# Kernel tuning notes

Hardware: AMD Instinct MI355X
Metric: run time of the kernel (lower is better)

The kernel has to match this reference:

```python
import jax, jax.numpy as jnp
import numpy as np

N = 50000
E = 800000
F_IN = 256
HID = 64
HEADS = 4
CLASSES = 32
NEG_SLOPE = 0.2


def setup_inputs() -> dict:
    key = jax.random.key(0)
    ks = jax.random.split(key, 10)
    x = jax.random.normal(ks[0], (N, F_IN), dtype=jnp.float32)
    edge_index = jax.random.randint(ks[1], (2, E), 0, N, dtype=jnp.int64)
    s1 = 1.0 / np.sqrt(F_IN)
    s2 = 1.0 / np.sqrt(HID * HEADS)
    W1 = jax.random.normal(ks[2], (F_IN, HEADS * HID), dtype=jnp.float32) * s1
    a_src1 = jax.random.normal(ks[3], (HEADS, HID), dtype=jnp.float32) * s1
    a_dst1 = jax.random.normal(ks[4], (HEADS, HID), dtype=jnp.float32) * s1
    b1 = jnp.zeros((HEADS * HID,), dtype=jnp.float32)
    W2 = jax.random.normal(ks[5], (HEADS * HID, CLASSES), dtype=jnp.float32) * s2
    a_src2 = jax.random.normal(ks[6], (1, CLASSES), dtype=jnp.float32) * s2
    a_dst2 = jax.random.normal(ks[7], (1, CLASSES), dtype=jnp.float32) * s2
    b2 = jnp.zeros((CLASSES,), dtype=jnp.float32)
    return {"x": x, "edge_index": edge_index, "W1": W1, "a_src1": a_src1,
            "a_dst1": a_dst1, "b1": b1, "W2": W2, "a_src2": a_src2,
            "a_dst2": a_dst2, "b2": b2}


def gat_conv(x, src, dst, W, a_src, a_dst, bias, num_nodes):
    # PyG GATConv: h = x W, per-head attention logits, segment softmax over dst,
    # scatter-weighted aggregation. src/dst already include self-loops.
    H, C = a_src.shape
    h = (x @ W).reshape(num_nodes, H, C)               # [N, H, C]
    al_s = jnp.sum(h * a_src[None], axis=-1)            # [N, H]
    al_d = jnp.sum(h * a_dst[None], axis=-1)            # [N, H]
    e = jax.nn.leaky_relu(al_s[src] + al_d[dst], NEG_SLOPE)  # [Et, H]
    m = jax.ops.segment_max(e, dst, num_segments=num_nodes)  # [N, H]
    ex = jnp.exp(e - m[dst])
    denom = jax.ops.segment_sum(ex, dst, num_segments=num_nodes)
    alpha = ex / denom[dst]                              # [Et, H]
    out = jax.ops.segment_sum(alpha[:, :, None] * h[src], dst,
                              num_segments=num_nodes)    # [N, H, C]
    return out.reshape(num_nodes, H * C) + bias


def reference(x, edge_index, W1, a_src1, a_dst1, b1, W2, a_src2, a_dst2, b2):
    num_nodes = x.shape[0]
    loop = jnp.arange(num_nodes, dtype=edge_index.dtype)
    src = jnp.concatenate([edge_index[0], loop])  # add_self_loops=True (PyG default)
    dst = jnp.concatenate([edge_index[1], loop])
    # dropout is identity in eval mode
    h = jax.nn.elu(gat_conv(x, src, dst, W1, a_src1, a_dst1, b1, num_nodes))
    out = gat_conv(h, src, dst, W2, a_src2, a_dst2, b2, num_nodes)
    return jax.nn.log_softmax(out, axis=1)
```

## Files before the change

kernel.cpp:

```cpp
#include <hip/hip_runtime.h>
#include <math.h>

#define N_NODES 50000
#define N_EDGES 800000
#define NEG_SLOPE 0.2f
#define PADU N_NODES
#define LOG2E 1.44269504088896f

#define BSHIFT 8
#define NBUK ((N_NODES + 255) >> BSHIFT)
#define BCAP 4608
#define ACHUNK 4096
#define PADBUK 5632
#define ET_PAD_ALLOC (NBUK * PADBUK)

typedef __attribute__((ext_vector_type(8))) short s16x8;
typedef __attribute__((ext_vector_type(4))) float f32x4;
typedef __attribute__((ext_vector_type(2))) float f32x2;

__device__ __forceinline__ unsigned short f2bf(float f) {
    union { float f; unsigned u; } v; v.f = f;
    unsigned r = v.u + 0x7FFF + ((v.u >> 16) & 1);
    return (unsigned short)(r >> 16);
}
__device__ __forceinline__ float asf(unsigned u) {
    union { unsigned u; float f; } v; v.u = u;
    return v.f;
}
__device__ __forceinline__ uint4 pack_bf16_trunc(float4 f0, float4 f1) {
    const unsigned* a = (const unsigned*)&f0;
    const unsigned* b = (const unsigned*)&f1;
    uint4 r;
    r.x = (a[0] >> 16) | (a[1] & 0xffff0000u);
    r.y = (a[2] >> 16) | (a[3] & 0xffff0000u);
    r.z = (b[0] >> 16) | (b[1] & 0xffff0000u);
    r.w = (b[2] >> 16) | (b[3] & 0xffff0000u);
    return r;
}
__device__ __forceinline__ unsigned char f2fp8(float f) {
    return (unsigned char)(__builtin_amdgcn_cvt_pk_fp8_f32(f, f, 0, false) & 0xff);
}


__global__ __launch_bounds__(256) void k_cvtw(const float* __restrict__ W1, const float* __restrict__ W2,
                                              unsigned short* __restrict__ WT, unsigned short* __restrict__ W2T,
                                              int* __restrict__ bcur, float* __restrict__ als1,
                                              unsigned char* __restrict__ H8) {
    int b = blockIdx.x, k = threadIdx.x;
    if (b < 256) {
        WT[b * 256 + k] = f2bf(W1[k * 256 + b]);
    } else if (b < 288) {
        int c = b - 256;
        W2T[c * 256 + k] = f2bf(W2[k * 32 + c]);
    } else {
        if (k < NBUK) bcur[k] = 0;
        if (k >= 196 && k < 200) als1[N_NODES * 4 + (k - 196)] = -1e30f;
        if (k >= 200 && k < 264) ((unsigned*)H8)[(size_t)N_NODES * 64 + (k - 200)] = 0;
    }
}


__global__ __launch_bounds__(256) void k_bin(const int* __restrict__ ei, int* __restrict__ bcur,
                                             unsigned* __restrict__ stage) {
    __shared__ unsigned sdata[ACHUNK];
    __shared__ unsigned short sv[ACHUNK];
    __shared__ int scnt[NBUK];
    __shared__ int soff[NBUK + 1];
    __shared__ int sgbase[NBUK];
    __shared__ int wssc[4];
    int tid = threadIdx.x;
    int e0 = blockIdx.x * ACHUNK;
    int nE = N_EDGES - e0;
    if (nE > ACHUNK) nE = ACHUNK;
    for (int i = tid; i < NBUK; i += 256) scnt[i] = 0;
    __syncthreads();
    for (int i = tid; i < nE; i += 256) {
        int v = ei[N_EDGES + e0 + i];
        sv[i] = (unsigned short)v;
        atomicAdd(&scnt[v >> BSHIFT], 1);
    }
    __syncthreads();
    {
        int lane = tid & 63, w = tid >> 6;
        int val = (tid < NBUK) ? scnt[tid] : 0;
        int incl = val;
        for (int o = 1; o < 64; o <<= 1) {
            int t = __shfl_up(incl, o);
            if (lane >= o) incl += t;
        }
        if (lane == 63) wssc[w] = incl;
        __syncthreads();
        int wb = 0;
        for (int i = 0; i < w; ++i) wb += wssc[i];
        if (tid < NBUK) soff[tid] = wb + incl - val;
        if (tid == 255) soff[NBUK] = wb + incl;
    }
    __syncthreads();
    if (tid < NBUK) {
        int c = scnt[tid];
        sgbase[tid] = c ? atomicAdd(&bcur[tid], c) : 0;
        scnt[tid] = soff[tid];
    }
    __syncthreads();
    for (int i = tid; i < nE; i += 256) {
        int u = ei[e0 + i];
        unsigned v = sv[i];
        int b = (int)(v >> BSHIFT);
        int pos = atomicAdd(&scnt[b], 1);
        sdata[pos] = (unsigned)u | ((v & 255u) << 16) | ((unsigned)b << 24);
    }
    __syncthreads();
    for (int i = tid; i < nE; i += 256) {
        unsigned pk = sdata[i];
        int buk = (int)(pk >> 24);
        int rel = sgbase[buk] + (i - soff[buk]);
        if (rel < BCAP) stage[(size_t)buk * BCAP + rel] = pk;
    }
}


__global__ __launch_bounds__(256) void k_build(const unsigned* __restrict__ stage,
                                               const int* __restrict__ bcur,
                                               int* __restrict__ offp, int* __restrict__ ecnt,
                                               unsigned short* __restrict__ esrc) {
    __shared__ int hist[256];
    __shared__ int lexcl[257];
    __shared__ int ws[4];
    __shared__ int outbuf[PADBUK];
    int b = blockIdx.x, tid = threadIdx.x;
    int n = bcur[b];
    if (n > BCAP) n = BCAP;
    int base = b << BSHIFT;
    int nv = N_NODES - base;
    if (nv > 256) nv = 256;
    hist[tid] = 0;
    __syncthreads();
    const unsigned* sg = stage + (size_t)b * BCAP;
    for (int i = tid; i < n; i += 256) atomicAdd(&hist[(sg[i] >> 16) & 0xFF], 1);
    __syncthreads();
    int lane = tid & 63, w = tid >> 6;
    int c = (tid < nv) ? hist[tid] + 1 : 0;
    int r = (tid < nv) ? ((c + 3) & ~3) : 0;
    int incl = r;
    for (int o = 1; o < 64; o <<= 1) {
        int t = __shfl_up(incl, o);
        if (lane >= o) incl += t;
    }
    if (lane == 63) ws[w] = incl;
    __syncthreads();
    int wb = 0;
    for (int i = 0; i < w; ++i) wb += ws[i];
    int excl = wb + incl - r;
    lexcl[tid] = excl;
    if (tid == 255) lexcl[256] = excl + r;
    int gb = b * PADBUK;
    if (tid < nv) {
        offp[base + tid] = gb + excl;
        ecnt[base + tid] = c;
    }
    __syncthreads();
    int total = lexcl[256];
    if (tid < nv) {
        outbuf[excl] = base + tid;
        for (int j = excl + c; j < excl + r; ++j) outbuf[j] = PADU;
        hist[tid] = 1;
    }
    __syncthreads();
    for (int i = tid; i < n; i += 256) {
        unsigned pk = sg[i];
        int vloc = (int)((pk >> 16) & 0xFF);
        int pos = lexcl[vloc] + atomicAdd(&hist[vloc], 1);
        outbuf[pos] = (int)(pk & 0xffffu);
    }
    __syncthreads();
    for (int i = tid; i < total; i += 256) esrc[gb + i] = (unsigned short)outbuf[i];
}


__global__ __launch_bounds__(256) void k_gemm1m(const float* __restrict__ X, const unsigned short* __restrict__ WT,
                                                const float* __restrict__ a_src, const float* __restrict__ a_dst,
                                                unsigned char* __restrict__ H8,
                                                float* __restrict__ als, float* __restrict__ ald) {
    __shared__ unsigned short As[64][40];
    __shared__ unsigned short Bs[256][40];
    int tid = threadIdx.x;
    int row0 = blockIdx.x * 64;
    int wv = tid >> 6, lane = tid & 63;
    int wm = wv & 1, wn = wv >> 1;
    int lr = lane & 15, quad = lane >> 4;
    f32x4 acc[2][8];
#pragma unroll
    for (int mt = 0; mt < 2; ++mt)
#pragma unroll
        for (int nt = 0; nt < 8; ++nt) acc[mt][nt] = (f32x4){0.f, 0.f, 0.f, 0.f};

    int ar = tid >> 2, aseg = tid & 3;
    for (int k0 = 0; k0 < 256; k0 += 32) {
        {
            int grow = row0 + ar;
            float4 f0 = make_float4(0.f, 0.f, 0.f, 0.f), f1 = f0;
            if (grow < N_NODES) {
                const float* src = X + (size_t)grow * 256 + k0 + aseg * 8;
                f0 = *(const float4*)src;
                f1 = *(const float4*)(src + 4);
            }
            *(uint4*)&As[ar][aseg * 8] = pack_bf16_trunc(f0, f1);
        }
#pragma unroll
        for (int pass = 0; pass < 4; ++pass) {
            int q = tid + pass * 256;
            int n = q >> 2, seg = q & 3;
            uint4 v = *(const uint4*)(WT + (n << 8) + k0 + seg * 8);
            *(uint4*)&Bs[n][seg * 8] = v;
        }
        __syncthreads();
        s16x8 a[2], b[8];
#pragma unroll
        for (int mt = 0; mt < 2; ++mt) a[mt] = *(const s16x8*)&As[wm * 32 + mt * 16 + lr][quad * 8];
#pragma unroll
        for (int nt = 0; nt < 8; ++nt) b[nt] = *(const s16x8*)&Bs[wn * 128 + nt * 16 + lr][quad * 8];
#pragma unroll
        for (int mt = 0; mt < 2; ++mt)
#pragma unroll
            for (int nt = 0; nt < 8; ++nt)
                acc[mt][nt] = __builtin_amdgcn_mfma_f32_16x16x32_bf16(a[mt], b[nt], acc[mt][nt], 0, 0, 0);
        __syncthreads();
    }
#pragma unroll
    for (int mt = 0; mt < 2; ++mt) {
#pragma unroll
        for (int r = 0; r < 4; ++r) {
            int row = row0 + wm * 32 + mt * 16 + quad * 4 + r;
            if (row < N_NODES) {
#pragma unroll
                for (int nt = 0; nt < 8; ++nt) {
                    int col = wn * 128 + nt * 16 + lr;
                    H8[(size_t)row * 256 + col] = f2fp8(acc[mt][nt][r]);
                }
            }
        }
    }
    float av[8], dv[8];
#pragma unroll
    for (int nt = 0; nt < 8; ++nt) {
        int col = wn * 128 + nt * 16 + lr;
        av[nt] = a_src[col] * LOG2E;
        dv[nt] = a_dst[col] * LOG2E;
    }
    float ps[2][8], pd[2][8];
#pragma unroll
    for (int hl = 0; hl < 2; ++hl)
#pragma unroll
        for (int i = 0; i < 8; ++i) { ps[hl][i] = 0.f; pd[hl][i] = 0.f; }
#pragma unroll
    for (int mt = 0; mt < 2; ++mt)
#pragma unroll
        for (int nt = 0; nt < 8; ++nt) {
            int hl = nt >> 2;
#pragma unroll
            for (int r = 0; r < 4; ++r) {
                float v = acc[mt][nt][r];
                ps[hl][mt * 4 + r] = fmaf(v, av[nt], ps[hl][mt * 4 + r]);
                pd[hl][mt * 4 + r] = fmaf(v, dv[nt], pd[hl][mt * 4 + r]);
            }
        }
#pragma unroll
    for (int hl = 0; hl < 2; ++hl)
#pragma unroll
        for (int i = 0; i < 8; ++i) {
            float s = ps[hl][i], d = pd[hl][i];
#pragma unroll
            for (int m = 8; m >= 1; m >>= 1) { s += __shfl_xor(s, m); d += __shfl_xor(d, m); }
            if (lr == 0) {
                int row = row0 + wm * 32 + (i >> 2) * 16 + quad * 4 + (i & 3);
                if (row < N_NODES) {
                    als[row * 4 + wn * 2 + hl] = s;
                    ald[row * 4 + wn * 2 + hl] = d;
                }
            }
        }
}


__global__ __launch_bounds__(256) void k_agg1(const uint2* __restrict__ H8u2,
                                              const float* __restrict__ als, const float* __restrict__ ald_,
                                              const int* __restrict__ offp, const int* __restrict__ ecnt,
                                              const unsigned short* __restrict__ esrc,
                                              const float* __restrict__ b1, uint2* __restrict__ H2p2) {
    int tid = threadIdx.x;
    int wid = (blockIdx.x * 256 + tid) >> 6;
    int half = (tid >> 5) & 1;
    int node = wid * 2 + half;
    int lane = tid & 31;
    int head = lane >> 3;
    float ald = ald_[node * 4 + head];
    int pstart = offp[node];
    int rend = pstart + ((ecnt[node] + 3) & ~3);
    float l = 0.f;
    f32x2 acc0 = (f32x2){0.f, 0.f}, acc1 = (f32x2){0.f, 0.f};
    f32x2 acc2 = (f32x2){0.f, 0.f}, acc3 = (f32x2){0.f, 0.f};

    auto quad = [&](unsigned ua, unsigned ub) {
        int u0 = (int)(ua & 0xffffu), u1 = (int)(ua >> 16);
        int u2 = (int)(ub & 0xffffu), u3 = (int)(ub >> 16);
        uint2 v0 = H8u2[(unsigned)u0 * 32 + lane];
        uint2 v1 = H8u2[(unsigned)u1 * 32 + lane];
        uint2 v2 = H8u2[(unsigned)u2 * 32 + lane];
        uint2 v3 = H8u2[(unsigned)u3 * 32 + lane];
        f32x2 e01 = (f32x2){als[u0 * 4 + head], als[u1 * 4 + head]} + (f32x2){ald, ald};
        f32x2 e23 = (f32x2){als[u2 * 4 + head], als[u3 * 4 + head]} + (f32x2){ald, ald};
        f32x2 t01 = e01 * NEG_SLOPE, t23 = e23 * NEG_SLOPE;
        float e0 = fmaxf(e01.x, t01.x), e1 = fmaxf(e01.y, t01.y);
        float e2 = fmaxf(e23.x, t23.x), e3 = fmaxf(e23.y, t23.y);
        float pw0 = __builtin_amdgcn_exp2f(e0);
        float pw1 = __builtin_amdgcn_exp2f(e1);
        float pw2 = __builtin_amdgcn_exp2f(e2);
        float pw3 = __builtin_amdgcn_exp2f(e3);
        l += (pw0 + pw1) + (pw2 + pw3);
        f32x2 w0 = (f32x2){pw0, pw0}, w1 = (f32x2){pw1, pw1};
        f32x2 w2 = (f32x2){pw2, pw2}, w3 = (f32x2){pw3, pw3};
        acc0 += w0 * __builtin_amdgcn_cvt_pk_f32_fp8(v0.x, false);
        acc1 += w0 * __builtin_amdgcn_cvt_pk_f32_fp8(v0.x, true);
        acc2 += w0 * __builtin_amdgcn_cvt_pk_f32_fp8(v0.y, false);
        acc3 += w0 * __builtin_amdgcn_cvt_pk_f32_fp8(v0.y, true);
        acc0 += w1 * __builtin_amdgcn_cvt_pk_f32_fp8(v1.x, false);
        acc1 += w1 * __builtin_amdgcn_cvt_pk_f32_fp8(v1.x, true);
        acc2 += w1 * __builtin_amdgcn_cvt_pk_f32_fp8(v1.y, false);
        acc3 += w1 * __builtin_amdgcn_cvt_pk_f32_fp8(v1.y, true);
        acc0 += w2 * __builtin_amdgcn_cvt_pk_f32_fp8(v2.x, false);
        acc1 += w2 * __builtin_amdgcn_cvt_pk_f32_fp8(v2.x, true);
        acc2 += w2 * __builtin_amdgcn_cvt_pk_f32_fp8(v2.y, false);
        acc3 += w2 * __builtin_amdgcn_cvt_pk_f32_fp8(v2.y, true);
        acc0 += w3 * __builtin_amdgcn_cvt_pk_f32_fp8(v3.x, false);
        acc1 += w3 * __builtin_amdgcn_cvt_pk_f32_fp8(v3.x, true);
        acc2 += w3 * __builtin_amdgcn_cvt_pk_f32_fp8(v3.y, false);
        acc3 += w3 * __builtin_amdgcn_cvt_pk_f32_fp8(v3.y, true);
    };

    int p = pstart;
    for (; p + 7 < rend; p += 8) {
        uint2 ua = *(const uint2*)(esrc + p);
        uint2 ub = *(const uint2*)(esrc + p + 4);
        quad(ua.x, ua.y);
        quad(ub.x, ub.y);
    }
    if (p < rend) {
        uint2 ua = *(const uint2*)(esrc + p);
        quad(ua.x, ua.y);
    }

    float inv = 1.f / l;
    int c = lane * 8;
    float4 bb0 = *(const float4*)(b1 + c);
    float4 bb1 = *(const float4*)(b1 + c + 4);
    float o0 = acc0.x * inv + bb0.x, o1 = acc0.y * inv + bb0.y;
    float o2 = acc1.x * inv + bb0.z, o3 = acc1.y * inv + bb0.w;
    float o4 = acc2.x * inv + bb1.x, o5 = acc2.y * inv + bb1.y;
    float o6 = acc3.x * inv + bb1.z, o7 = acc3.y * inv + bb1.w;
    o0 = o0 > 0.f ? o0 : expm1f(o0);
    o1 = o1 > 0.f ? o1 : expm1f(o1);
    o2 = o2 > 0.f ? o2 : expm1f(o2);
    o3 = o3 > 0.f ? o3 : expm1f(o3);
    o4 = o4 > 0.f ? o4 : expm1f(o4);
    o5 = o5 > 0.f ? o5 : expm1f(o5);
    o6 = o6 > 0.f ? o6 : expm1f(o6);
    o7 = o7 > 0.f ? o7 : expm1f(o7);
    unsigned pkx = __builtin_amdgcn_cvt_pk_fp8_f32(o0, o1, 0, false);
    pkx = __builtin_amdgcn_cvt_pk_fp8_f32(o2, o3, pkx, true);
    unsigned pky = __builtin_amdgcn_cvt_pk_fp8_f32(o4, o5, 0, false);
    pky = __builtin_amdgcn_cvt_pk_fp8_f32(o6, o7, pky, true);
    H2p2[(unsigned)node * 32 + lane] = make_uint2(pkx, pky);
}


__global__ __launch_bounds__(256) void k_gemm2m(const unsigned* __restrict__ H2p,
                                                const unsigned short* __restrict__ W2T,
                                                const float* __restrict__ as2, const float* __restrict__ ad2,
                                                unsigned short* __restrict__ Gb, float* __restrict__ als2,
                                                float* __restrict__ ald2) {
    int tid = threadIdx.x;
    int wv = tid >> 6, lane = tid & 63, lr = lane & 15, quad = lane >> 4;
    int row0 = blockIdx.x * 64 + wv * 16;
    int rowA = row0 + lr;
    unsigned rA = (rowA < N_NODES) ? (unsigned)rowA : (unsigned)(N_NODES - 1);
    f32x4 acc[2];
    acc[0] = (f32x4){0.f, 0.f, 0.f, 0.f};
    acc[1] = (f32x4){0.f, 0.f, 0.f, 0.f};
#pragma unroll
    for (int k0 = 0; k0 < 256; k0 += 32) {
        uint2 d = *(const uint2*)(H2p + rA * 64 + (k0 >> 2) + quad * 2);
        f32x2 f0 = __builtin_amdgcn_cvt_pk_f32_fp8(d.x, false);
        f32x2 f1 = __builtin_amdgcn_cvt_pk_f32_fp8(d.x, true);
        f32x2 f2 = __builtin_amdgcn_cvt_pk_f32_fp8(d.y, false);
        f32x2 f3 = __builtin_amdgcn_cvt_pk_f32_fp8(d.y, true);
        union { uint4 u; s16x8 s; } cv;
        cv.u = pack_bf16_trunc(make_float4(f0.x, f0.y, f1.x, f1.y), make_float4(f2.x, f2.y, f3.x, f3.y));
        s16x8 afrag = cv.s;
        s16x8 b0 = *(const s16x8*)(W2T + lr * 256 + k0 + quad * 8);
        s16x8 b1f = *(const s16x8*)(W2T + (16 + lr) * 256 + k0 + quad * 8);
        acc[0] = __builtin_amdgcn_mfma_f32_16x16x32_bf16(afrag, b0, acc[0], 0, 0, 0);
        acc[1] = __builtin_amdgcn_mfma_f32_16x16x32_bf16(afrag, b1f, acc[1], 0, 0, 0);
    }
    float a2s = as2[lr] * LOG2E, a2s2 = as2[16 + lr] * LOG2E;
    float a2d = ad2[lr] * LOG2E, a2d2 = ad2[16 + lr] * LOG2E;
#pragma unroll
    for (int r = 0; r < 4; ++r) {
        int row = row0 + quad * 4 + r;
        float g0 = acc[0][r], g1 = acc[1][r];
        float s = g0 * a2s + g1 * a2s2;
        float dd = g0 * a2d + g1 * a2d2;
#pragma unroll
        for (int m = 8; m >= 1; m >>= 1) { s += __shfl_xor(s, m); dd += __shfl_xor(dd, m); }
        if (row < N_NODES) {
            Gb[(size_t)row * 32 + lr] = f2bf(g0);
            Gb[(size_t)row * 32 + 16 + lr] = f2bf(g1);
            if (lr == 0) { als2[row] = s; ald2[row] = dd; }
        }
    }
}


__global__ __launch_bounds__(256) void k_agg2(const unsigned short* __restrict__ Gb,
                                              const float* __restrict__ als2,
                                              const float* __restrict__ ald2_, const int* __restrict__ offp,
                                              const int* __restrict__ ecnt,
                                              const unsigned short* __restrict__ esrc, const float* __restrict__ b2,
                                              float* __restrict__ out) {
    int gid = blockIdx.x * 256 + threadIdx.x;
    int node = gid >> 4;
    int colp = gid & 15;
    if (node >= N_NODES) return;
    float ald = ald2_[node];
    int pstart = offp[node];
    int pend = pstart + ecnt[node];
    float l = 0.f;
    f32x2 accv = (f32x2){0.f, 0.f};

    auto edge1 = [&](int u0) {
        unsigned gpk = *(const unsigned*)(Gb + (size_t)(unsigned)u0 * 32 + 2 * colp);
        f32x2 g01 = (f32x2){asf(gpk << 16), asf(gpk & 0xffff0000u)};
        float e0 = als2[u0] + ald;
        e0 = fmaxf(e0, NEG_SLOPE * e0);
        float pw0 = __builtin_amdgcn_exp2f(e0);
        l += pw0;
        accv += (f32x2){pw0, pw0} * g01;
    };
    auto quad = [&](unsigned ua, unsigned ub) {
        int u0 = (int)(ua & 0xffffu), u1 = (int)(ua >> 16);
        int u2 = (int)(ub & 0xffffu), u3 = (int)(ub >> 16);
        unsigned g0p = *(const unsigned*)(Gb + (size_t)(unsigned)u0 * 32 + 2 * colp);
        unsigned g1p = *(const unsigned*)(Gb + (size_t)(unsigned)u1 * 32 + 2 * colp);
        unsigned g2p = *(const unsigned*)(Gb + (size_t)(unsigned)u2 * 32 + 2 * colp);
        unsigned g3p = *(const unsigned*)(Gb + (size_t)(unsigned)u3 * 32 + 2 * colp);
        f32x2 e01 = (f32x2){als2[u0], als2[u1]} + (f32x2){ald, ald};
        f32x2 e23 = (f32x2){als2[u2], als2[u3]} + (f32x2){ald, ald};
        f32x2 t01 = e01 * NEG_SLOPE, t23 = e23 * NEG_SLOPE;
        float e0 = fmaxf(e01.x, t01.x), e1 = fmaxf(e01.y, t01.y);
        float e2 = fmaxf(e23.x, t23.x), e3 = fmaxf(e23.y, t23.y);
        float pw0 = __builtin_amdgcn_exp2f(e0), pw1 = __builtin_amdgcn_exp2f(e1);
        float pw2 = __builtin_amdgcn_exp2f(e2), pw3 = __builtin_amdgcn_exp2f(e3);
        l += (pw0 + pw1) + (pw2 + pw3);
        f32x2 g0 = (f32x2){asf(g0p << 16), asf(g0p & 0xffff0000u)};
        f32x2 g1 = (f32x2){asf(g1p << 16), asf(g1p & 0xffff0000u)};
        f32x2 g2 = (f32x2){asf(g2p << 16), asf(g2p & 0xffff0000u)};
        f32x2 g3 = (f32x2){asf(g3p << 16), asf(g3p & 0xffff0000u)};
        accv += (f32x2){pw0, pw0} * g0;
        accv += (f32x2){pw1, pw1} * g1;
        accv += (f32x2){pw2, pw2} * g2;
        accv += (f32x2){pw3, pw3} * g3;
    };

    int p = pstart;
    for (; p + 7 < pend; p += 8) {
        uint2 ua = *(const uint2*)(esrc + p);
        uint2 ub = *(const uint2*)(esrc + p + 4);
        quad(ua.x, ua.y);
        quad(ub.x, ub.y);
    }
    for (; p + 3 < pend; p += 4) {
        uint2 ua = *(const uint2*)(esrc + p);
        quad(ua.x, ua.y);
    }
    for (; p < pend; ++p) edge1(esrc[p]);

    float inv = 1.f / l;
    float2 bb = *(const float2*)(b2 + 2 * colp);
    float o0 = accv.x * inv + bb.x;
    float o1 = accv.y * inv + bb.y;
    float mm = fmaxf(o0, o1);
#pragma unroll
    for (int msk = 8; msk >= 1; msk >>= 1) mm = fmaxf(mm, __shfl_xor(mm, msk));
    float s = __expf(o0 - mm) + __expf(o1 - mm);
#pragma unroll
    for (int msk = 8; msk >= 1; msk >>= 1) s += __shfl_xor(s, msk);
    float ls = logf(s);
    float2 res = make_float2(o0 - mm - ls, o1 - mm - ls);
    *(float2*)(out + (size_t)node * 32 + 2 * colp) = res;
}


extern "C" void kernel_launch(void* const* d_in, const int* in_sizes, int n_in,
                              void* d_out, int out_size, void* d_ws, size_t ws_size,
                              hipStream_t stream) {
    const float* x   = (const float*)d_in[0];
    const int*   ei  = (const int*)d_in[1];
    const float* W1  = (const float*)d_in[2];
    const float* as1 = (const float*)d_in[3];
    const float* ad1 = (const float*)d_in[4];
    const float* b1  = (const float*)d_in[5];
    const float* W2  = (const float*)d_in[6];
    const float* as2 = (const float*)d_in[7];
    const float* ad2 = (const float*)d_in[8];
    const float* b2  = (const float*)d_in[9];
    float* out = (float*)d_out;

    char* p = (char*)d_ws;
    auto alloc = [&](size_t bytes) {
        char* r = p;
        p += (bytes + 255) & ~(size_t)255;
        return r;
    };
    unsigned char*  h8  = (unsigned char*)alloc((size_t)(N_NODES + 1) * 256);
    unsigned char*  h2pr= (unsigned char*)alloc((size_t)N_NODES * 64 * 4);
    unsigned short* wt  = (unsigned short*)alloc((size_t)256 * 256 * 2);
    unsigned short* w2t = (unsigned short*)alloc((size_t)32 * 256 * 2);
    float* als1 = (float*)alloc(((size_t)N_NODES * 4 + 4) * 4);
    float* ald1 = (float*)alloc((size_t)N_NODES * 4 * 4);
    float* als2 = (float*)alloc((size_t)N_NODES * 4);
    float* ald2 = (float*)alloc((size_t)N_NODES * 4);
    int* bcur    = (int*)alloc(256 * 4);
    int* offp = (int*)alloc((size_t)N_NODES * 4);
    int* ecnt = (int*)alloc((size_t)N_NODES * 4);
    unsigned short* esrc = (unsigned short*)alloc((size_t)ET_PAD_ALLOC * 2);

    unsigned* stage = (unsigned*)h2pr;
    unsigned* h2p = (unsigned*)h2pr;
    unsigned short* g = (unsigned short*)h8;

    k_cvtw<<<289, 256, 0, stream>>>(W1, W2, wt, w2t, bcur, als1, h8);
    k_bin<<<(N_EDGES + ACHUNK - 1) / ACHUNK, 256, 0, stream>>>(ei, bcur, stage);
    k_build<<<NBUK, 256, 0, stream>>>(stage, bcur, offp, ecnt, esrc);

    k_gemm1m<<<(N_NODES + 63) / 64, 256, 0, stream>>>(x, wt, as1, ad1, h8, als1, ald1);
    k_agg1<<<(N_NODES / 2 + 3) / 4, 256, 0, stream>>>((const uint2*)h8, als1, ald1, offp, ecnt, esrc, b1,
                                                      (uint2*)h2p);
    k_gemm2m<<<(N_NODES + 63) / 64, 256, 0, stream>>>(h2p, w2t, as2, ad2, g, als2, ald2);
    k_agg2<<<(N_NODES * 16 + 255) / 256, 256, 0, stream>>>(g, als2, ald2, offp, ecnt, esrc, b2, out);
}
```

Measured before the change: 216.3 us.

## Merge independent preprocessing kernels into two launches via block-range dispatch

Folds weight conversion into the edge-binning kernel, and the layer-1 GEMM together with the CSR build into a second kernel, so each block picks its role from its block index. Zeroing the bucket counters moves to a hipMemsetAsync. This cuts the launch count from four to two plus a memset, and lets independent work overlap inside a single grid. The cost is a larger shared-memory union for the combined kernel, which may lower occupancy for the GEMM blocks. The GEMM reads the converted weights, but those are written by the previous kernel, so stream ordering still holds.

```diff
diff --git a/kernel.cpp b/kernel.cpp
--- a/kernel.cpp
+++ b/kernel.cpp
@@ -11,8 +11,10 @@
 #define NBUK ((N_NODES + 255) >> BSHIFT)
 #define BCAP 4608
 #define ACHUNK 4096
+#define BINB ((N_EDGES + ACHUNK - 1) / ACHUNK)
 #define PADBUK 5632
 #define ET_PAD_ALLOC (NBUK * PADBUK)
+#define G1B ((N_NODES + 63) / 64)
 
 typedef __attribute__((ext_vector_type(8))) short s16x8;
 typedef __attribute__((ext_vector_type(4))) float f32x4;
@@ -42,26 +44,11 @@
 }
 
 
-__global__ __launch_bounds__(256) void k_cvtw(const float* __restrict__ W1, const float* __restrict__ W2,
+__global__ __launch_bounds__(256) void k_pre1(const int* __restrict__ ei, int* __restrict__ bcur,
+                                              unsigned* __restrict__ stage,
+                                              const float* __restrict__ W1, const float* __restrict__ W2,
                                               unsigned short* __restrict__ WT, unsigned short* __restrict__ W2T,
-                                              int* __restrict__ bcur, float* __restrict__ als1,
-                                              unsigned char* __restrict__ H8) {
-    int b = blockIdx.x, k = threadIdx.x;
-    if (b < 256) {
-        WT[b * 256 + k] = f2bf(W1[k * 256 + b]);
-    } else if (b < 288) {
-        int c = b - 256;
-        W2T[c * 256 + k] = f2bf(W2[k * 32 + c]);
-    } else {
-        if (k < NBUK) bcur[k] = 0;
-        if (k >= 196 && k < 200) als1[N_NODES * 4 + (k - 196)] = -1e30f;
-        if (k >= 200 && k < 264) ((unsigned*)H8)[(size_t)N_NODES * 64 + (k - 200)] = 0;
-    }
-}
-
-
-__global__ __launch_bounds__(256) void k_bin(const int* __restrict__ ei, int* __restrict__ bcur,
-                                             unsigned* __restrict__ stage) {
+                                              float* __restrict__ als1, unsigned char* __restrict__ H8) {
     __shared__ unsigned sdata[ACHUNK];
     __shared__ unsigned short sv[ACHUNK];
     __shared__ int scnt[NBUK];
@@ -69,7 +56,24 @@
     __shared__ int sgbase[NBUK];
     __shared__ int wssc[4];
     int tid = threadIdx.x;
-    int e0 = blockIdx.x * ACHUNK;
+    int blk = blockIdx.x;
+
+    if (blk >= BINB) {
+        int b = blk - BINB;
+        int k = tid;
+        if (b < 256) {
+            WT[b * 256 + k] = f2bf(W1[k * 256 + b]);
+        } else if (b < 288) {
+            int c = b - 256;
+            W2T[c * 256 + k] = f2bf(W2[k * 32 + c]);
+        } else {
+            if (k >= 196 && k < 200) als1[N_NODES * 4 + (k - 196)] = -1e30f;
+            if (k >= 200 && k < 264) ((unsigned*)H8)[(size_t)N_NODES * 64 + (k - 200)] = 0;
+        }
+        return;
+    }
+
+    int e0 = blk * ACHUNK;
     int nE = N_EDGES - e0;
     if (nE > ACHUNK) nE = ACHUNK;
     for (int i = tid; i < NBUK; i += 256) scnt[i] = 0;
@@ -119,15 +123,123 @@
 }
 
 
-__global__ __launch_bounds__(256) void k_build(const unsigned* __restrict__ stage,
-                                               const int* __restrict__ bcur,
-                                               int* __restrict__ offp, int* __restrict__ ecnt,
-                                               unsigned short* __restrict__ esrc) {
-    __shared__ int hist[256];
-    __shared__ int lexcl[257];
-    __shared__ int ws[4];
-    __shared__ int outbuf[PADBUK];
-    int b = blockIdx.x, tid = threadIdx.x;
+__global__ __launch_bounds__(256) void k_pre2(const float* __restrict__ X, const unsigned short* __restrict__ WT,
+                                              const float* __restrict__ a_src, const float* __restrict__ a_dst,
+                                              unsigned char* __restrict__ H8,
+                                              float* __restrict__ als, float* __restrict__ ald,
+                                              const unsigned* __restrict__ stage, const int* __restrict__ bcur,
+                                              int* __restrict__ offp, int* __restrict__ ecnt,
+                                              unsigned short* __restrict__ esrc) {
+    __shared__ int smraw_i[6400];
+    char* smraw = (char*)smraw_i;
+    int tid = threadIdx.x;
+
+    if (blockIdx.x < G1B) {
+        unsigned short (*As)[40] = (unsigned short(*)[40])smraw;
+        unsigned short (*Bs)[40] = (unsigned short(*)[40])(smraw + 5120);
+        int row0 = blockIdx.x * 64;
+        int wv = tid >> 6, lane = tid & 63;
+        int wm = wv & 1, wn = wv >> 1;
+        int lr = lane & 15, quad = lane >> 4;
+        f32x4 acc[2][8];
+#pragma unroll
+        for (int mt = 0; mt < 2; ++mt)
+#pragma unroll
+            for (int nt = 0; nt < 8; ++nt) acc[mt][nt] = (f32x4){0.f, 0.f, 0.f, 0.f};
+
+        int ar = tid >> 2, aseg = tid & 3;
+        for (int k0 = 0; k0 < 256; k0 += 32) {
+            {
+                int grow = row0 + ar;
+                float4 f0 = make_float4(0.f, 0.f, 0.f, 0.f), f1 = f0;
+                if (grow < N_NODES) {
+                    const float* src = X + (size_t)grow * 256 + k0 + aseg * 8;
+                    f0 = *(const float4*)src;
+                    f1 = *(const float4*)(src + 4);
+                }
+                *(uint4*)&As[ar][aseg * 8] = pack_bf16_trunc(f0, f1);
+            }
+#pragma unroll
+            for (int pass = 0; pass < 4; ++pass) {
+                int q = tid + pass * 256;
+                int n = q >> 2, seg = q & 3;
+                uint4 v = *(const uint4*)(WT + (n << 8) + k0 + seg * 8);
+                *(uint4*)&Bs[n][seg * 8] = v;
+            }
+            __syncthreads();
+            s16x8 a[2], b[8];
+#pragma unroll
+            for (int mt = 0; mt < 2; ++mt) a[mt] = *(const s16x8*)&As[wm * 32 + mt * 16 + lr][quad * 8];
+#pragma unroll
+            for (int nt = 0; nt < 8; ++nt) b[nt] = *(const s16x8*)&Bs[wn * 128 + nt * 16 + lr][quad * 8];
+#pragma unroll
+            for (int mt = 0; mt < 2; ++mt)
+#pragma unroll
+                for (int nt = 0; nt < 8; ++nt)
+                    acc[mt][nt] = __builtin_amdgcn_mfma_f32_16x16x32_bf16(a[mt], b[nt], acc[mt][nt], 0, 0, 0);
+            __syncthreads();
+        }
+#pragma unroll
+        for (int mt = 0; mt < 2; ++mt) {
+#pragma unroll
+            for (int r = 0; r < 4; ++r) {
+                int row = row0 + wm * 32 + mt * 16 + quad * 4 + r;
+                if (row < N_NODES) {
+#pragma unroll
+                    for (int nt = 0; nt < 8; ++nt) {
+                        int col = wn * 128 + nt * 16 + lr;
+                        H8[(size_t)row * 256 + col] = f2fp8(acc[mt][nt][r]);
+                    }
+                }
+            }
+        }
+        float av[8], dv[8];
+#pragma unroll
+        for (int nt = 0; nt < 8; ++nt) {
+            int col = wn * 128 + nt * 16 + lr;
+            av[nt] = a_src[col] * LOG2E;
+            dv[nt] = a_dst[col] * LOG2E;
+        }
+        float ps[2][8], pd[2][8];
+#pragma unroll
+        for (int hl = 0; hl < 2; ++hl)
+#pragma unroll
+            for (int i = 0; i < 8; ++i) { ps[hl][i] = 0.f; pd[hl][i] = 0.f; }
+#pragma unroll
+        for (int mt = 0; mt < 2; ++mt)
+#pragma unroll
+            for (int nt = 0; nt < 8; ++nt) {
+                int hl = nt >> 2;
+#pragma unroll
+                for (int r = 0; r < 4; ++r) {
+                    float v = acc[mt][nt][r];
+                    ps[hl][mt * 4 + r] = fmaf(v, av[nt], ps[hl][mt * 4 + r]);
+                    pd[hl][mt * 4 + r] = fmaf(v, dv[nt], pd[hl][mt * 4 + r]);
+                }
+            }
+#pragma unroll
+        for (int hl = 0; hl < 2; ++hl)
+#pragma unroll
+            for (int i = 0; i < 8; ++i) {
+                float s = ps[hl][i], d = pd[hl][i];
+#pragma unroll
+                for (int m = 8; m >= 1; m >>= 1) { s += __shfl_xor(s, m); d += __shfl_xor(d, m); }
+                if (lr == 0) {
+                    int row = row0 + wm * 32 + (i >> 2) * 16 + quad * 4 + (i & 3);
+                    if (row < N_NODES) {
+                        als[row * 4 + wn * 2 + hl] = s;
+                        ald[row * 4 + wn * 2 + hl] = d;
+                    }
+                }
+            }
+        return;
+    }
+
+    int* hist   = (int*)smraw;
+    int* lexcl  = (int*)(smraw + 1024);
+    int* ws     = (int*)(smraw + 2052);
+    int* outbuf = (int*)(smraw + 2068);
+    int b = blockIdx.x - G1B;
     int n = bcur[b];
     if (n > BCAP) n = BCAP;
     int base = b << BSHIFT;
@@ -174,111 +286,6 @@
     }
     __syncthreads();
     for (int i = tid; i < total; i += 256) esrc[gb + i] = (unsigned short)outbuf[i];
-}
-
-
-__global__ __launch_bounds__(256) void k_gemm1m(const float* __restrict__ X, const unsigned short* __restrict__ WT,
-                                                const float* __restrict__ a_src, const float* __restrict__ a_dst,
-                                                unsigned char* __restrict__ H8,
-                                                float* __restrict__ als, float* __restrict__ ald) {
-    __shared__ unsigned short As[64][40];
-    __shared__ unsigned short Bs[256][40];
-    int tid = threadIdx.x;
-    int row0 = blockIdx.x * 64;
-    int wv = tid >> 6, lane = tid & 63;
-    int wm = wv & 1, wn = wv >> 1;
-    int lr = lane & 15, quad = lane >> 4;
-    f32x4 acc[2][8];
-#pragma unroll
-    for (int mt = 0; mt < 2; ++mt)
-#pragma unroll
-        for (int nt = 0; nt < 8; ++nt) acc[mt][nt] = (f32x4){0.f, 0.f, 0.f, 0.f};
-
-    int ar = tid >> 2, aseg = tid & 3;
-    for (int k0 = 0; k0 < 256; k0 += 32) {
-        {
-            int grow = row0 + ar;
-            float4 f0 = make_float4(0.f, 0.f, 0.f, 0.f), f1 = f0;
-            if (grow < N_NODES) {
-                const float* src = X + (size_t)grow * 256 + k0 + aseg * 8;
-                f0 = *(const float4*)src;
-                f1 = *(const float4*)(src + 4);
-            }
-            *(uint4*)&As[ar][aseg * 8] = pack_bf16_trunc(f0, f1);
-        }
-#pragma unroll
-        for (int pass = 0; pass < 4; ++pass) {
-            int q = tid + pass * 256;
-            int n = q >> 2, seg = q & 3;
-            uint4 v = *(const uint4*)(WT + (n << 8) + k0 + seg * 8);
-            *(uint4*)&Bs[n][seg * 8] = v;
-        }
-        __syncthreads();
-        s16x8 a[2], b[8];
-#pragma unroll
-        for (int mt = 0; mt < 2; ++mt) a[mt] = *(const s16x8*)&As[wm * 32 + mt * 16 + lr][quad * 8];
-#pragma unroll
-        for (int nt = 0; nt < 8; ++nt) b[nt] = *(const s16x8*)&Bs[wn * 128 + nt * 16 + lr][quad * 8];
-#pragma unroll
-        for (int mt = 0; mt < 2; ++mt)
-#pragma unroll
-            for (int nt = 0; nt < 8; ++nt)
-                acc[mt][nt] = __builtin_amdgcn_mfma_f32_16x16x32_bf16(a[mt], b[nt], acc[mt][nt], 0, 0, 0);
-        __syncthreads();
-    }
-#pragma unroll
-    for (int mt = 0; mt < 2; ++mt) {
-#pragma unroll
-        for (int r = 0; r < 4; ++r) {
-            int row = row0 + wm * 32 + mt * 16 + quad * 4 + r;
-            if (row < N_NODES) {
-#pragma unroll
-                for (int nt = 0; nt < 8; ++nt) {
-                    int col = wn * 128 + nt * 16 + lr;
-                    H8[(size_t)row * 256 + col] = f2fp8(acc[mt][nt][r]);
-                }
-            }
-        }
-    }
-    float av[8], dv[8];
-#pragma unroll
-    for (int nt = 0; nt < 8; ++nt) {
-        int col = wn * 128 + nt * 16 + lr;
-        av[nt] = a_src[col] * LOG2E;
-        dv[nt] = a_dst[col] * LOG2E;
-    }
-    float ps[2][8], pd[2][8];
-#pragma unroll
-    for (int hl = 0; hl < 2; ++hl)
-#pragma unroll
-        for (int i = 0; i < 8; ++i) { ps[hl][i] = 0.f; pd[hl][i] = 0.f; }
-#pragma unroll
-    for (int mt = 0; mt < 2; ++mt)
-#pragma unroll
-        for (int nt = 0; nt < 8; ++nt) {
-            int hl = nt >> 2;
-#pragma unroll
-            for (int r = 0; r < 4; ++r) {
-                float v = acc[mt][nt][r];
-                ps[hl][mt * 4 + r] = fmaf(v, av[nt], ps[hl][mt * 4 + r]);
-                pd[hl][mt * 4 + r] = fmaf(v, dv[nt], pd[hl][mt * 4 + r]);
-            }
-        }
-#pragma unroll
-    for (int hl = 0; hl < 2; ++hl)
-#pragma unroll
-        for (int i = 0; i < 8; ++i) {
-            float s = ps[hl][i], d = pd[hl][i];
-#pragma unroll
-            for (int m = 8; m >= 1; m >>= 1) { s += __shfl_xor(s, m); d += __shfl_xor(d, m); }
-            if (lr == 0) {
-                int row = row0 + wm * 32 + (i >> 2) * 16 + quad * 4 + (i & 3);
-                if (row < N_NODES) {
-                    als[row * 4 + wn * 2 + hl] = s;
-                    ald[row * 4 + wn * 2 + hl] = d;
-                }
-            }
-        }
 }
 
 
@@ -537,11 +544,9 @@
     unsigned* h2p = (unsigned*)h2pr;
     unsigned short* g = (unsigned short*)h8;
 
-    k_cvtw<<<289, 256, 0, stream>>>(W1, W2, wt, w2t, bcur, als1, h8);
-    k_bin<<<(N_EDGES + ACHUNK - 1) / ACHUNK, 256, 0, stream>>>(ei, bcur, stage);
-    k_build<<<NBUK, 256, 0, stream>>>(stage, bcur, offp, ecnt, esrc);
-
-    k_gemm1m<<<(N_NODES + 63) / 64, 256, 0, stream>>>(x, wt, as1, ad1, h8, als1, ald1);
+    hipMemsetAsync(bcur, 0, 256 * 4, stream);
+    k_pre1<<<BINB + 289, 256, 0, stream>>>(ei, bcur, stage, W1, W2, wt, w2t, als1, h8);
+    k_pre2<<<G1B + NBUK, 256, 0, stream>>>(x, wt, as1, ad1, h8, als1, ald1, stage, bcur, offp, ecnt, esrc);
     k_agg1<<<(N_NODES / 2 + 3) / 4, 256, 0, stream>>>((const uint2*)h8, als1, ald1, offp, ecnt, esrc, b1,
                                                       (uint2*)h2p);
     k_gemm2m<<<(N_NODES + 63) / 64, 256, 0, stream>>>(h2p, w2t, as2, ad2, g, als2, ald2);
```

Result: faster. 207.8 us, median of 2 (-3.9%).
